# Kernel optimization log

Measured on AMD Instinct MI355X. Metric: run time of the kernel, lower is better.

Reference implementation:

```python
import jax, jax.numpy as jnp
import numpy as np
import math

B, S, E, H = 4, 2048, 512, 8
DK = E // H
NEG = -1000000000.0


def setup_inputs() -> dict:
    key = jax.random.key(0)
    ks = jax.random.split(key, 12)
    std = 1.0 / math.sqrt(E)
    inp = {
        "query": jax.random.normal(ks[0], (B, S, E), dtype=jnp.float32),
        "key_in": jax.random.normal(ks[1], (B, S, E), dtype=jnp.float32),
        "value": jax.random.normal(ks[2], (B, S, E), dtype=jnp.float32),
        "mask": jax.random.randint(ks[3], (B, S, S), 0, 2, dtype=jnp.int32),
        "Wq": jax.random.normal(ks[4], (E, E), dtype=jnp.float32) * std,
        "bq": jnp.zeros((E,), dtype=jnp.float32),
        "Wk": jax.random.normal(ks[5], (E, E), dtype=jnp.float32) * std,
        "bk": jnp.zeros((E,), dtype=jnp.float32),
        "Wv": jax.random.normal(ks[6], (E, E), dtype=jnp.float32) * std,
        "bv": jnp.zeros((E,), dtype=jnp.float32),
        "Wo": jax.random.normal(ks[7], (E, E), dtype=jnp.float32) * std,
        "bo": jnp.zeros((E,), dtype=jnp.float32),
    }
    return inp


def reference(query, key_in, value, mask, Wq, bq, Wk, bk, Wv, bv, Wo, bo):
    # Linear projections (torch nn.Linear: x @ W.T + b)
    q = (query @ Wq.T + bq).reshape(B, S, H, DK).transpose(0, 2, 1, 3)   # [B,H,S,dk]
    k = (key_in @ Wk.T + bk).reshape(B, S, H, DK).transpose(0, 2, 1, 3)
    v = (value @ Wv.T + bv).reshape(B, S, H, DK).transpose(0, 2, 1, 3)
    # Faithful quirk: scores MULTIPLIED by sqrt(dk), as in the source
    scores = jnp.einsum("bhqd,bhkd->bhqk", q, k) * math.sqrt(DK)
    scores = jnp.where(mask[:, None, :, :] == 0, NEG, scores)
    attn = jax.nn.softmax(scores, axis=-1)
    out = jnp.einsum("bhqk,bhkd->bhqd", attn, v)                         # [B,H,S,dk]
    # Faithful quirk: direct view [B,H,S,dk] -> [B,S,E] WITHOUT head transpose
    out = out.reshape(B, S, E)
    return out @ Wo.T + bo
```

## Files before the change

kernel.cpp:

```cpp
#include <hip/hip_runtime.h>

#define BB 4
#define SS 2048
#define EE 512
#define HH 8
#define DKK 64
#define MM (BB*SS)

typedef unsigned short u16;
typedef unsigned int u32;
typedef unsigned long long u64;
typedef __attribute__((ext_vector_type(8))) short short8;
typedef __attribute__((ext_vector_type(4))) short short4v;
typedef __attribute__((ext_vector_type(4))) float f32x4;

__device__ inline u16 f2bf(float f) {
  union { float f; u32 u; } v; v.f = f;
  u32 r = v.u + 0x7fff + ((v.u >> 16) & 1);
  return (u16)(r >> 16);
}
__device__ inline float bf2f(u16 u) {
  union { u32 u; float f; } v; v.u = ((u32)u) << 16;
  return v.f;
}
__device__ inline void split2(float f, u16 &h, u16 &l) {
  h = f2bf(f);
  l = f2bf(f - bf2f(h));
}

template<int CTRL>
__device__ inline float fdpp(float x) {
  return __builtin_bit_cast(float,
      __builtin_amdgcn_update_dpp(0, __builtin_bit_cast(int, x), CTRL, 0xf, 0xf, true));
}
__device__ inline float rmax16(float x) {
  x = fmaxf(x, fdpp<0x121>(x));
  x = fmaxf(x, fdpp<0x122>(x));
  x = fmaxf(x, fdpp<0x124>(x));
  x = fmaxf(x, fdpp<0x128>(x));
  return x;
}
__device__ inline float rsum16(float x) {
  x += fdpp<0x121>(x);
  x += fdpp<0x122>(x);
  x += fdpp<0x124>(x);
  x += fdpp<0x128>(x);
  return x;
}

__global__ __launch_bounds__(256) void maskpack(const int* __restrict__ mask,
                                                u64* __restrict__ mb) {
  const int bq = blockIdx.x;
  const int w = threadIdx.x >> 6, l = threadIdx.x & 63;
  const int* src = mask + (size_t)bq * SS;
  #pragma unroll
  for (int it = 0; it < 8; ++it) {
    int tb = it * 4 + w;
    int m = src[tb * 64 + l];
    u64 bits = __ballot(m != 0);
    if (l == 0) mb[(size_t)bq * 32 + tb] = bits;
  }
}

template<int COMP>
__global__ __launch_bounds__(256) void proj(
    const float* __restrict__ A, const float* __restrict__ W,
    const float* __restrict__ bias, u16* __restrict__ Chi, u16* __restrict__ Clo,
    float cscale)
{
  __shared__ __align__(16) u16 Ah[128][72];
  __shared__ __align__(16) u16 Al[COMP ? 128 : 1][72];
  __shared__ __align__(16) u16 Bh[64][72];
  __shared__ __align__(16) u16 Bl[COMP ? 64 : 1][72];
  const int m0 = blockIdx.x * 128, n0 = blockIdx.y * 64;
  const int tid = threadIdx.x, w = tid >> 6, l = tid & 63;
  const int row = l & 15, kq = (l >> 4) * 8;
  f32x4 acc[2][4];
  #pragma unroll
  for (int i = 0; i < 2; ++i)
    #pragma unroll
    for (int j = 0; j < 4; ++j) acc[i][j] = (f32x4){0.f, 0.f, 0.f, 0.f};

  for (int k0 = 0; k0 < 512; k0 += 64) {
    __syncthreads();
    #pragma unroll
    for (int i = 0; i < 8; ++i) {
      int u = tid + i * 256; int r = u >> 4, c4 = (u & 15) * 4;
      f32x4 v = *(const f32x4*)&A[(size_t)(m0 + r) * 512 + k0 + c4];
      u16 h[4], lo[4];
      #pragma unroll
      for (int j = 0; j < 4; ++j) split2(v[j], h[j], lo[j]);
      *(short4v*)&Ah[r][c4] = (short4v){(short)h[0], (short)h[1], (short)h[2], (short)h[3]};
      if (COMP)
        *(short4v*)&Al[r][c4] = (short4v){(short)lo[0], (short)lo[1], (short)lo[2], (short)lo[3]};
    }
    #pragma unroll
    for (int i = 0; i < 4; ++i) {
      int u = tid + i * 256; int r = u >> 4, c4 = (u & 15) * 4;
      f32x4 v = *(const f32x4*)&W[(size_t)(n0 + r) * 512 + k0 + c4];
      u16 h[4], lo[4];
      #pragma unroll
      for (int j = 0; j < 4; ++j) split2(v[j], h[j], lo[j]);
      *(short4v*)&Bh[r][c4] = (short4v){(short)h[0], (short)h[1], (short)h[2], (short)h[3]};
      if (COMP)
        *(short4v*)&Bl[r][c4] = (short4v){(short)lo[0], (short)lo[1], (short)lo[2], (short)lo[3]};
    }
    __syncthreads();
    short8 ah[2][2], al[2][2], bh[4][2], bl[4][2];
    #pragma unroll
    for (int mf = 0; mf < 2; ++mf)
      #pragma unroll
      for (int ks = 0; ks < 2; ++ks) {
        ah[mf][ks] = *(const short8*)&Ah[w * 32 + mf * 16 + row][ks * 32 + kq];
        if (COMP) al[mf][ks] = *(const short8*)&Al[w * 32 + mf * 16 + row][ks * 32 + kq];
      }
    #pragma unroll
    for (int nf = 0; nf < 4; ++nf)
      #pragma unroll
      for (int ks = 0; ks < 2; ++ks) {
        bh[nf][ks] = *(const short8*)&Bh[nf * 16 + row][ks * 32 + kq];
        if (COMP) bl[nf][ks] = *(const short8*)&Bl[nf * 16 + row][ks * 32 + kq];
      }
    #pragma unroll
    for (int mf = 0; mf < 2; ++mf)
      #pragma unroll
      for (int nf = 0; nf < 4; ++nf)
        #pragma unroll
        for (int ks = 0; ks < 2; ++ks) {
          acc[mf][nf] = __builtin_amdgcn_mfma_f32_16x16x32_bf16(
              ah[mf][ks], bh[nf][ks], acc[mf][nf], 0, 0, 0);
          if (COMP) {
            acc[mf][nf] = __builtin_amdgcn_mfma_f32_16x16x32_bf16(
                ah[mf][ks], bl[nf][ks], acc[mf][nf], 0, 0, 0);
            acc[mf][nf] = __builtin_amdgcn_mfma_f32_16x16x32_bf16(
                al[mf][ks], bh[nf][ks], acc[mf][nf], 0, 0, 0);
          }
        }
  }
  #pragma unroll
  for (int mf = 0; mf < 2; ++mf)
    #pragma unroll
    for (int nf = 0; nf < 4; ++nf)
      #pragma unroll
      for (int r = 0; r < 4; ++r) {
        int m = m0 + w * 32 + mf * 16 + ((l >> 4) << 2) + r;
        int n = n0 + nf * 16 + (l & 15);
        float c = (acc[mf][nf][r] + bias[n]) * cscale;
        size_t idx = (size_t)m * 512 + n;
        if (COMP) { u16 h, lo; split2(c, h, lo); Chi[idx] = h; Clo[idx] = lo; }
        else Chi[idx] = f2bf(c);
      }
}

__global__ __launch_bounds__(256) void gemm_out(
    const u16* __restrict__ A, const float* __restrict__ W,
    const float* __restrict__ bias, float* __restrict__ C)
{
  __shared__ __align__(16) u16 As[128][72];
  __shared__ __align__(16) u16 Bs[64][72];
  const int m0 = blockIdx.x * 128, n0 = blockIdx.y * 64;
  const int tid = threadIdx.x, w = tid >> 6, l = tid & 63;
  const int row = l & 15, kq = (l >> 4) * 8;
  f32x4 acc[2][4];
  #pragma unroll
  for (int i = 0; i < 2; ++i)
    #pragma unroll
    for (int j = 0; j < 4; ++j) acc[i][j] = (f32x4){0.f, 0.f, 0.f, 0.f};

  for (int k0 = 0; k0 < 512; k0 += 64) {
    __syncthreads();
    #pragma unroll
    for (int i = 0; i < 4; ++i) {
      int u = tid + i * 256; int r = u >> 3, c = (u & 7) * 8;
      *(short8*)&As[r][c] = *(const short8*)&A[(size_t)(m0 + r) * 512 + k0 + c];
    }
    #pragma unroll
    for (int i = 0; i < 4; ++i) {
      int u = tid + i * 256; int r = u >> 4, c4 = (u & 15) * 4;
      f32x4 v = *(const f32x4*)&W[(size_t)(n0 + r) * 512 + k0 + c4];
      *(short4v*)&Bs[r][c4] = (short4v){(short)f2bf(v[0]), (short)f2bf(v[1]),
                                        (short)f2bf(v[2]), (short)f2bf(v[3])};
    }
    __syncthreads();
    short8 a[2][2], bfr[4][2];
    #pragma unroll
    for (int mf = 0; mf < 2; ++mf)
      #pragma unroll
      for (int ks = 0; ks < 2; ++ks)
        a[mf][ks] = *(const short8*)&As[w * 32 + mf * 16 + row][ks * 32 + kq];
    #pragma unroll
    for (int nf = 0; nf < 4; ++nf)
      #pragma unroll
      for (int ks = 0; ks < 2; ++ks)
        bfr[nf][ks] = *(const short8*)&Bs[nf * 16 + row][ks * 32 + kq];
    #pragma unroll
    for (int mf = 0; mf < 2; ++mf)
      #pragma unroll
      for (int nf = 0; nf < 4; ++nf)
        #pragma unroll
        for (int ks = 0; ks < 2; ++ks)
          acc[mf][nf] = __builtin_amdgcn_mfma_f32_16x16x32_bf16(
              a[mf][ks], bfr[nf][ks], acc[mf][nf], 0, 0, 0);
  }
  #pragma unroll
  for (int mf = 0; mf < 2; ++mf)
    #pragma unroll
    for (int nf = 0; nf < 4; ++nf)
      #pragma unroll
      for (int r = 0; r < 4; ++r) {
        int m = m0 + w * 32 + mf * 16 + ((l >> 4) << 2) + r;
        int n = n0 + nf * 16 + (l & 15);
        C[(size_t)m * 512 + n] = acc[mf][nf][r] + bias[n];
      }
}

__global__ __launch_bounds__(256) void attn(
    const u16* __restrict__ Qhi, const u16* __restrict__ Qlo,
    const u16* __restrict__ Khi, const u16* __restrict__ Klo,
    const u16* __restrict__ V, const u64* __restrict__ MB,
    u16* __restrict__ X)
{
  __shared__ __align__(16) u16 KhiS[64][64];
  __shared__ __align__(16) u16 KloS[64][64];
  __shared__ __align__(16) u16 VtS[64][64];
  __shared__ __align__(16) u16 Pl[64][64];
  const int b = blockIdx.z, h = blockIdx.y, q0 = blockIdx.x * 64;
  const int tid = threadIdx.x, w = tid >> 6, l = tid & 63;
  const int row = l & 15, kq = (l >> 4) * 8;
  const int r0 = tid >> 3;
  const int c0 = (tid & 7) * 8;

  const size_t qbase = ((size_t)(b * SS) + q0 + w * 16 + row) * EE + h * DKK;
  short8 qh[2], ql[2];
  #pragma unroll
  for (int ks = 0; ks < 2; ++ks) {
    qh[ks] = *(const short8*)&Qhi[qbase + ks * 32 + kq];
    ql[ks] = *(const short8*)&Qlo[qbase + ks * 32 + kq];
  }

  float mrow[4], lrow[4];
  f32x4 acco[4];
  #pragma unroll
  for (int r = 0; r < 4; ++r) { mrow[r] = -INFINITY; lrow[r] = 0.f; }
  #pragma unroll
  for (int f = 0; f < 4; ++f) acco[f] = (f32x4){0.f, 0.f, 0.f, 0.f};

  const int qr0 = q0 + w * 16 + ((l >> 4) << 2);
  const size_t mbase = ((size_t)(b * SS) + qr0) * 32;

  short8 sh[2], sl[2], sv[2];
  u64 wb[4], wbn[4];

  #pragma unroll
  for (int i = 0; i < 2; ++i) {
    size_t g = ((size_t)(b * SS) + r0 + 32 * i) * EE + h * DKK + c0;
    sh[i] = *(const short8*)&Khi[g];
    sl[i] = *(const short8*)&Klo[g];
    sv[i] = *(const short8*)&V[g];
  }
  #pragma unroll
  for (int r = 0; r < 4; ++r) wb[r] = MB[mbase + r * 32] >> (l & 15);
  #pragma unroll
  for (int i = 0; i < 2; ++i) {
    int rr = r0 + 32 * i;
    int kc = c0 ^ ((rr & 7) << 3);
    *(short8*)&KhiS[rr][kc] = sh[i];
    *(short8*)&KloS[rr][kc] = sl[i];
    #pragma unroll
    for (int j = 0; j < 8; ++j) {
      int d = c0 + j;
      VtS[d][rr ^ (((d & 7) ^ (d >> 3)) << 3)] = (u16)sv[i][j];
    }
  }
  __syncthreads();

  for (int t0 = 0; t0 < SS; t0 += 64) {
    const bool more = (t0 + 64 < SS);
    if (more) {
      #pragma unroll
      for (int i = 0; i < 2; ++i) {
        size_t g = ((size_t)(b * SS) + t0 + 64 + r0 + 32 * i) * EE + h * DKK + c0;
        sh[i] = *(const short8*)&Khi[g];
        sl[i] = *(const short8*)&Klo[g];
        sv[i] = *(const short8*)&V[g];
      }
      #pragma unroll
      for (int r = 0; r < 4; ++r)
        wbn[r] = MB[mbase + r * 32 + ((t0 >> 6) + 1)] >> (l & 15);
    }

    f32x4 sacc[4];
    #pragma unroll
    for (int f = 0; f < 4; ++f) sacc[f] = (f32x4){0.f, 0.f, 0.f, 0.f};
    #pragma unroll
    for (int f = 0; f < 4; ++f) {
      int krow = f * 16 + row;
      int ksw = (krow & 7) << 3;
      #pragma unroll
      for (int ks = 0; ks < 2; ++ks) {
        short8 kh = *(const short8*)&KhiS[krow][(ks * 32 + kq) ^ ksw];
        short8 kl = *(const short8*)&KloS[krow][(ks * 32 + kq) ^ ksw];
        sacc[f] = __builtin_amdgcn_mfma_f32_16x16x32_bf16(qh[ks], kh, sacc[f], 0, 0, 0);
        sacc[f] = __builtin_amdgcn_mfma_f32_16x16x32_bf16(qh[ks], kl, sacc[f], 0, 0, 0);
        sacc[f] = __builtin_amdgcn_mfma_f32_16x16x32_bf16(ql[ks], kh, sacc[f], 0, 0, 0);
      }
    }

    float sval[4][4];
    #pragma unroll
    for (int f = 0; f < 4; ++f)
      #pragma unroll
      for (int r = 0; r < 4; ++r)
        sval[f][r] = ((wb[r] >> (16 * f)) & 1ULL) ? sacc[f][r] : -1e9f;

    #pragma unroll
    for (int r = 0; r < 4; ++r) {
      float mx = fmaxf(fmaxf(sval[0][r], sval[1][r]), fmaxf(sval[2][r], sval[3][r]));
      mx = rmax16(mx);
      float mnew = fmaxf(mrow[r], mx);
      float alpha = __expf(mrow[r] - mnew);
      float rs = 0.f;
      #pragma unroll
      for (int f = 0; f < 4; ++f) {
        float p = __expf(sval[f][r] - mnew);
        sval[f][r] = p; rs += p;
      }
      rs = rsum16(rs);
      lrow[r] = lrow[r] * alpha + rs;
      mrow[r] = mnew;
      #pragma unroll
      for (int f = 0; f < 4; ++f) acco[f][r] *= alpha;
    }

    #pragma unroll
    for (int f = 0; f < 4; ++f)
      #pragma unroll
      for (int r = 0; r < 4; ++r) {
        int rr = ((l >> 4) << 2) + r;
        Pl[w * 16 + rr][(f * 16 + (l & 15)) ^ (((rr & 7) ^ (rr >> 3)) << 3)] = f2bf(sval[f][r]);
      }

    {
      int psw = ((row & 7) ^ (row >> 3)) << 3;
      #pragma unroll
      for (int f2 = 0; f2 < 4; ++f2) {
        int d = f2 * 16 + row;
        int vsw = ((d & 7) ^ (d >> 3)) << 3;
        #pragma unroll
        for (int ks = 0; ks < 2; ++ks) {
          short8 p = *(const short8*)&Pl[w * 16 + row][(ks * 32 + kq) ^ psw];
          short8 vvf = *(const short8*)&VtS[d][(ks * 32 + kq) ^ vsw];
          acco[f2] = __builtin_amdgcn_mfma_f32_16x16x32_bf16(p, vvf, acco[f2], 0, 0, 0);
        }
      }
    }

    __syncthreads();
    if (more) {
      #pragma unroll
      for (int i = 0; i < 2; ++i) {
        int rr = r0 + 32 * i;
        int kc = c0 ^ ((rr & 7) << 3);
        *(short8*)&KhiS[rr][kc] = sh[i];
        *(short8*)&KloS[rr][kc] = sl[i];
        #pragma unroll
        for (int j = 0; j < 8; ++j) {
          int d = c0 + j;
          VtS[d][rr ^ (((d & 7) ^ (d >> 3)) << 3)] = (u16)sv[i][j];
        }
      }
      #pragma unroll
      for (int r = 0; r < 4; ++r) wb[r] = wbn[r];
    }
    __syncthreads();
  }

  #pragma unroll
  for (int f2 = 0; f2 < 4; ++f2)
    #pragma unroll
    for (int r = 0; r < 4; ++r) {
      int q = q0 + w * 16 + ((l >> 4) << 2) + r;
      int d = f2 * 16 + (l & 15);
      float o = acco[f2][r] / lrow[r];
      int sp = h * 256 + (q >> 3);
      int ep = ((q & 7) << 6) + d;
      X[((size_t)(b * SS) + sp) * EE + ep] = f2bf(o);
    }
}

extern "C" void kernel_launch(void* const* d_in, const int* in_sizes, int n_in,
                              void* d_out, int out_size, void* d_ws, size_t ws_size,
                              hipStream_t stream) {
  const float* query  = (const float*)d_in[0];
  const float* key_in = (const float*)d_in[1];
  const float* value  = (const float*)d_in[2];
  const int*   mask   = (const int*)d_in[3];
  const float* Wq = (const float*)d_in[4];
  const float* bq = (const float*)d_in[5];
  const float* Wk = (const float*)d_in[6];
  const float* bk = (const float*)d_in[7];
  const float* Wv = (const float*)d_in[8];
  const float* bv = (const float*)d_in[9];
  const float* Wo = (const float*)d_in[10];
  const float* bo = (const float*)d_in[11];

  u16* ws = (u16*)d_ws;
  const size_t NE = (size_t)MM * EE;
  u16* Qhi = ws;
  u16* Qlo = ws + NE;
  u16* Khi = ws + 2 * NE;
  u16* Klo = ws + 3 * NE;
  u16* Vp  = ws + 4 * NE;
  u16* X   = ws + 5 * NE;
  u64* MBb = (u64*)(ws + 6 * NE);

  dim3 gblk(MM / 128, EE / 64);
  maskpack<<<MM, 256, 0, stream>>>(mask, MBb);
  proj<1><<<gblk, 256, 0, stream>>>(query,  Wq, bq, Qhi, Qlo, 8.0f);
  proj<1><<<gblk, 256, 0, stream>>>(key_in, Wk, bk, Khi, Klo, 1.0f);
  proj<0><<<gblk, 256, 0, stream>>>(value,  Wv, bv, Vp, nullptr, 1.0f);
  attn<<<dim3(SS / 64, HH, BB), 256, 0, stream>>>(Qhi, Qlo, Khi, Klo, Vp, MBb, X);
  gemm_out<<<gblk, 256, 0, stream>>>(X, Wo, bo, (float*)d_out);
}
```

Before: 394.1 us.

## Pre-split fp32 inputs and weights into bf16 hi/lo buffers before projection GEMMs

Adds a presplit kernel that converts activations and weights from fp32 into bf16 hi/lo pairs once, so the projection and output GEMMs load bf16 directly and skip per-tile conversion. Before, each weight tile was re-split by every M-block and each activation tile by every N-block. The cost is seven extra launches and an extra round trip through global memory for the inputs, which are written as bf16 and read back.

```diff
diff --git a/kernel.cpp b/kernel.cpp
--- a/kernel.cpp
+++ b/kernel.cpp
@@ -62,9 +62,27 @@
   }
 }
 
+template<int HAS_LO>
+__global__ __launch_bounds__(256) void presplit(const float* __restrict__ in,
+                                                u16* __restrict__ hi,
+                                                u16* __restrict__ lo, int n4) {
+  int idx = blockIdx.x * 256 + threadIdx.x;
+  const int stride = gridDim.x * 256;
+  for (; idx < n4; idx += stride) {
+    f32x4 v = *((const f32x4*)in + idx);
+    u16 h[4], l[4];
+    #pragma unroll
+    for (int j = 0; j < 4; ++j) split2(v[j], h[j], l[j]);
+    *((short4v*)hi + idx) = (short4v){(short)h[0], (short)h[1], (short)h[2], (short)h[3]};
+    if (HAS_LO)
+      *((short4v*)lo + idx) = (short4v){(short)l[0], (short)l[1], (short)l[2], (short)l[3]};
+  }
+}
+
 template<int COMP>
 __global__ __launch_bounds__(256) void proj(
-    const float* __restrict__ A, const float* __restrict__ W,
+    const u16* __restrict__ Ag, const u16* __restrict__ Alg,
+    const u16* __restrict__ Wg, const u16* __restrict__ Wlg,
     const float* __restrict__ bias, u16* __restrict__ Chi, u16* __restrict__ Clo,
     float cscale)
 {
@@ -84,26 +102,18 @@
   for (int k0 = 0; k0 < 512; k0 += 64) {
     __syncthreads();
     #pragma unroll
-    for (int i = 0; i < 8; ++i) {
-      int u = tid + i * 256; int r = u >> 4, c4 = (u & 15) * 4;
-      f32x4 v = *(const f32x4*)&A[(size_t)(m0 + r) * 512 + k0 + c4];
-      u16 h[4], lo[4];
-      #pragma unroll
-      for (int j = 0; j < 4; ++j) split2(v[j], h[j], lo[j]);
-      *(short4v*)&Ah[r][c4] = (short4v){(short)h[0], (short)h[1], (short)h[2], (short)h[3]};
+    for (int i = 0; i < 4; ++i) {
+      int u = tid + i * 256; int r = u >> 3, c = (u & 7) * 8;
+      *(short8*)&Ah[r][c] = *(const short8*)&Ag[(size_t)(m0 + r) * 512 + k0 + c];
       if (COMP)
-        *(short4v*)&Al[r][c4] = (short4v){(short)lo[0], (short)lo[1], (short)lo[2], (short)lo[3]};
-    }
-    #pragma unroll
-    for (int i = 0; i < 4; ++i) {
-      int u = tid + i * 256; int r = u >> 4, c4 = (u & 15) * 4;
-      f32x4 v = *(const f32x4*)&W[(size_t)(n0 + r) * 512 + k0 + c4];
-      u16 h[4], lo[4];
-      #pragma unroll
-      for (int j = 0; j < 4; ++j) split2(v[j], h[j], lo[j]);
-      *(short4v*)&Bh[r][c4] = (short4v){(short)h[0], (short)h[1], (short)h[2], (short)h[3]};
+        *(short8*)&Al[r][c] = *(const short8*)&Alg[(size_t)(m0 + r) * 512 + k0 + c];
+    }
+    #pragma unroll
+    for (int i = 0; i < 2; ++i) {
+      int u = tid + i * 256; int r = u >> 3, c = (u & 7) * 8;
+      *(short8*)&Bh[r][c] = *(const short8*)&Wg[(size_t)(n0 + r) * 512 + k0 + c];
       if (COMP)
-        *(short4v*)&Bl[r][c4] = (short4v){(short)lo[0], (short)lo[1], (short)lo[2], (short)lo[3]};
+        *(short8*)&Bl[r][c] = *(const short8*)&Wlg[(size_t)(n0 + r) * 512 + k0 + c];
     }
     __syncthreads();
     short8 ah[2][2], al[2][2], bh[4][2], bl[4][2];
@@ -153,7 +163,7 @@
 }
 
 __global__ __launch_bounds__(256) void gemm_out(
-    const u16* __restrict__ A, const float* __restrict__ W,
+    const u16* __restrict__ A, const u16* __restrict__ Wg,
     const float* __restrict__ bias, float* __restrict__ C)
 {
   __shared__ __align__(16) u16 As[128][72];
@@ -175,11 +185,9 @@
       *(short8*)&As[r][c] = *(const short8*)&A[(size_t)(m0 + r) * 512 + k0 + c];
     }
     #pragma unroll
-    for (int i = 0; i < 4; ++i) {
-      int u = tid + i * 256; int r = u >> 4, c4 = (u & 15) * 4;
-      f32x4 v = *(const f32x4*)&W[(size_t)(n0 + r) * 512 + k0 + c4];
-      *(short4v*)&Bs[r][c4] = (short4v){(short)f2bf(v[0]), (short)f2bf(v[1]),
-                                        (short)f2bf(v[2]), (short)f2bf(v[3])};
+    for (int i = 0; i < 2; ++i) {
+      int u = tid + i * 256; int r = u >> 3, c = (u & 7) * 8;
+      *(short8*)&Bs[r][c] = *(const short8*)&Wg[(size_t)(n0 + r) * 512 + k0 + c];
     }
     __syncthreads();
     short8 a[2][2], bfr[4][2];
@@ -406,19 +414,40 @@
 
   u16* ws = (u16*)d_ws;
   const size_t NE = (size_t)MM * EE;
+  const size_t WN = (size_t)EE * EE;
   u16* Qhi = ws;
   u16* Qlo = ws + NE;
   u16* Khi = ws + 2 * NE;
   u16* Klo = ws + 3 * NE;
   u16* Vp  = ws + 4 * NE;
-  u16* X   = ws + 5 * NE;
-  u64* MBb = (u64*)(ws + 6 * NE);
+  u16* Sh  = ws + 5 * NE;
+  u16* Sl  = ws + 6 * NE;
+  u16* X   = Sl;
+  u16* Wqh = ws + 7 * NE;
+  u16* Wql = Wqh + WN;
+  u16* Wkh = Wqh + 2 * WN;
+  u16* Wkl = Wqh + 3 * WN;
+  u16* Wvh = Wqh + 4 * WN;
+  u16* Woh = Wqh + 5 * WN;
+  u64* MBb = (u64*)(ws + 7 * NE + 6 * WN);
+
+  const int n4NE = (int)(NE / 4);
+  const int n4WN = (int)(WN / 4);
 
   dim3 gblk(MM / 128, EE / 64);
   maskpack<<<MM, 256, 0, stream>>>(mask, MBb);
-  proj<1><<<gblk, 256, 0, stream>>>(query,  Wq, bq, Qhi, Qlo, 8.0f);
-  proj<1><<<gblk, 256, 0, stream>>>(key_in, Wk, bk, Khi, Klo, 1.0f);
-  proj<0><<<gblk, 256, 0, stream>>>(value,  Wv, bv, Vp, nullptr, 1.0f);
+  presplit<1><<<256, 256, 0, stream>>>(Wq, Wqh, Wql, n4WN);
+  presplit<1><<<256, 256, 0, stream>>>(Wk, Wkh, Wkl, n4WN);
+  presplit<0><<<256, 256, 0, stream>>>(Wv, Wvh, nullptr, n4WN);
+  presplit<0><<<256, 256, 0, stream>>>(Wo, Woh, nullptr, n4WN);
+
+  presplit<1><<<2048, 256, 0, stream>>>(query, Sh, Sl, n4NE);
+  proj<1><<<gblk, 256, 0, stream>>>(Sh, Sl, Wqh, Wql, bq, Qhi, Qlo, 8.0f);
+  presplit<1><<<2048, 256, 0, stream>>>(key_in, Sh, Sl, n4NE);
+  proj<1><<<gblk, 256, 0, stream>>>(Sh, Sl, Wkh, Wkl, bk, Khi, Klo, 1.0f);
+  presplit<0><<<2048, 256, 0, stream>>>(value, Sh, nullptr, n4NE);
+  proj<0><<<gblk, 256, 0, stream>>>(Sh, nullptr, Wvh, nullptr, bv, Vp, nullptr, 1.0f);
+
   attn<<<dim3(SS / 64, HH, BB), 256, 0, stream>>>(Qhi, Qlo, Khi, Klo, Vp, MBb, X);
-  gemm_out<<<gblk, 256, 0, stream>>>(X, Wo, bo, (float*)d_out);
-}
+  gemm_out<<<gblk, 256, 0, stream>>>(X, Woh, bo, (float*)d_out);
+}
```

Measured after the change: 443.6 us. 1.13x slower.
